# Optimization experiments

Hardware: AMD Instinct MI355X
Metric: run time of the kernel (lower is better)

The kernel has to match this reference:

```python
import jax, jax.numpy as jnp
import numpy as np

T, B, D, H = 1024, 8, 1024, 16
HD = D // H  # head_dim = 64


def setup_inputs() -> dict:
    key = jax.random.key(0)
    ks = jax.random.split(key, 11)
    s = 1.0 / np.sqrt(D)
    return {
        "query": jax.random.normal(ks[0], (T, B, D), jnp.float32),
        "key": jax.random.normal(ks[1], (T, B, D), jnp.float32),
        "value": jax.random.normal(ks[2], (T, B, D), jnp.float32),
        "Wq": jax.random.normal(ks[3], (D, D), jnp.float32) * s,
        "bq": jax.random.normal(ks[4], (D,), jnp.float32) * s,
        "Wk": jax.random.normal(ks[5], (D, D), jnp.float32) * s,
        "bk": jax.random.normal(ks[6], (D,), jnp.float32) * s,
        "Wv": jax.random.normal(ks[7], (D, D), jnp.float32) * s,
        "bv": jax.random.normal(ks[8], (D,), jnp.float32) * s,
        "Wo": jax.random.normal(ks[9], (D, D), jnp.float32) * s,
        "bo": jax.random.normal(ks[10], (D,), jnp.float32) * s,
    }


def reference(query, key, value, Wq, bq, Wk, bk, Wv, bv, Wo, bo):
    # query/key/value: (T, B, D) seq-first, as in nn.MultiheadAttention
    t, b, d = query.shape
    scale = HD ** -0.5
    # projections (torch Linear: x @ W.T + b), split into heads -> (B, H, T, HD)
    q = (query @ Wq.T + bq).reshape(t, b, H, HD).transpose(1, 2, 0, 3)
    k = (key @ Wk.T + bk).reshape(t, b, H, HD).transpose(1, 2, 0, 3)
    v = (value @ Wv.T + bv).reshape(t, b, H, HD).transpose(1, 2, 0, 3)
    # full (B, H, T, T) scores, matching the module's explicit materialization
    attn = jnp.einsum('bhtd,bhsd->bhts', q, k) * scale
    attn = jax.nn.softmax(attn, axis=-1)
    # (B, H, T, HD) -> (T, B, D)
    out = jnp.einsum('bhts,bhsd->bhtd', attn, v)
    out = out.transpose(2, 0, 1, 3).reshape(t, b, d)
    return out @ Wo.T + bo
```

## Files before the change

### kernel.cpp

```cpp
#include <hip/hip_runtime.h>

#define T_SEQ 1024
#define BATCH 8
#define DMODEL 1024
#define NHEAD 16
#define HDIM 64
#define M_ROWS (T_SEQ * BATCH)
#define QSCALE (0.125f * 1.44269504088896f)

typedef unsigned short ushort_t;
typedef __attribute__((ext_vector_type(8))) short short8;
typedef __attribute__((ext_vector_type(4))) float f32x4;

#define G2L16(g, l) __builtin_amdgcn_global_load_lds(                      \
    (const __attribute__((address_space(1))) void*)(g),                    \
    (__attribute__((address_space(3))) void*)(l), 16, 0, 0)

static __device__ __forceinline__ ushort_t f2bf(float f) {
    unsigned int u = __builtin_bit_cast(unsigned int, f);
    u += 0x7FFFu + ((u >> 16) & 1u);
    return (ushort_t)(u >> 16);
}

#if __has_builtin(__builtin_amdgcn_cvt_pk_bf16_f32)
typedef __attribute__((ext_vector_type(2))) __bf16 bf16x2_t;
static __device__ __forceinline__ unsigned pk2(float lo, float hi) {
    bf16x2_t r = __builtin_amdgcn_cvt_pk_bf16_f32(lo, hi);
    return __builtin_bit_cast(unsigned, r);
}
#else
static __device__ __forceinline__ unsigned pk2(float lo, float hi) {
    return (unsigned)f2bf(lo) | ((unsigned)f2bf(hi) << 16);
}
#endif

#if __has_builtin(__builtin_amdgcn_exp2f)
#define EXP2F(x) __builtin_amdgcn_exp2f(x)
#else
#define EXP2F(x) exp2f(x)
#endif

__global__ __launch_bounds__(256) void cast3_bf16(
    const float4* __restrict__ a, const float4* __restrict__ b,
    const float4* __restrict__ c,
    uint2* __restrict__ oa, uint2* __restrict__ ob, uint2* __restrict__ oc,
    int n4)
{
    int i = blockIdx.x * 256 + threadIdx.x;
    if (i >= n4) return;
    const float4* src = (blockIdx.y == 0) ? a : (blockIdx.y == 1) ? b : c;
    uint2* dst        = (blockIdx.y == 0) ? oa : (blockIdx.y == 1) ? ob : oc;
    float4 v = src[i];
    uint2 o; o.x = pk2(v.x, v.y); o.y = pk2(v.z, v.w);
    dst[i] = o;
}

__global__ __launch_bounds__(256) void cast4_bf16(
    const float4* __restrict__ a, const float4* __restrict__ b,
    const float4* __restrict__ c, const float4* __restrict__ d,
    uint2* __restrict__ oa, uint2* __restrict__ ob,
    uint2* __restrict__ oc, uint2* __restrict__ od,
    int n4)
{
    int i = blockIdx.x * 256 + threadIdx.x;
    if (i >= n4) return;
    const float4* src = (blockIdx.y == 0) ? a : (blockIdx.y == 1) ? b
                      : (blockIdx.y == 2) ? c : d;
    uint2* dst        = (blockIdx.y == 0) ? oa : (blockIdx.y == 1) ? ob
                      : (blockIdx.y == 2) ? oc : od;
    float4 v = src[i];
    uint2 o; o.x = pk2(v.x, v.y); o.y = pk2(v.z, v.w);
    dst[i] = o;
}

template<bool OUT_BF16>
__global__ __launch_bounds__(256) void gemm_bt_mfma(
    const ushort_t* __restrict__ A, const ushort_t* __restrict__ Wbase,
    const float* __restrict__ bias0, const float* __restrict__ bias1,
    const float* __restrict__ bias2, void* __restrict__ Yv,
    int N, int K, float scale0)
{
    __shared__ ushort_t As[128 * 64];
    __shared__ ushort_t Bs[128 * 64];

    const int tid  = threadIdx.x;
    const int lane = tid & 63;
    const int quad = lane >> 4;
    const int l16  = lane & 15;
    const int w    = tid >> 6;
    const int wm   = w >> 1;
    const int wn   = w & 1;
    const int bn   = blockIdx.x;
    const int bmg  = blockIdx.y;

    const int sel = bmg >> 6;
    const ushort_t* Wb = Wbase + (size_t)sel * N * K;
    const float* bias = (sel == 0) ? bias0 : (sel == 1) ? bias1 : bias2;
    const float scale = (sel == 0) ? scale0 : 1.0f;

    const int srow_in = lane >> 3;
    const int sch     = lane & 7;

    const f32x4 zero4 = {0.f, 0.f, 0.f, 0.f};
    f32x4 acc[4][4];
#pragma unroll
    for (int i = 0; i < 4; i++)
#pragma unroll
        for (int j = 0; j < 4; j++) acc[i][j] = zero4;

    for (int k0 = 0; k0 < K; k0 += 64) {
        __syncthreads();
#pragma unroll
        for (int u = 0; u < 4; u++) {
            int seg = w * 4 + u;
            int row = seg * 8 + srow_in;
            int chs = sch ^ (row & 7);
            G2L16(&A [(size_t)(bmg * 128 + row) * K + k0 + chs * 8],
                  (char*)As + seg * 1024);
            G2L16(&Wb[(size_t)(bn  * 128 + row) * K + k0 + chs * 8],
                  (char*)Bs + seg * 1024);
        }
        __syncthreads();

#pragma unroll
        for (int ks = 0; ks < 2; ks++) {
            short8 af[4], bfr[4];
#pragma unroll
            for (int i = 0; i < 4; i++) {
                int row = wm * 64 + i * 16 + l16;
                af[i] = *(const short8*)&As[row * 64 + (((ks * 4 + quad) ^ (row & 7)) * 8)];
            }
#pragma unroll
            for (int j = 0; j < 4; j++) {
                int row = wn * 64 + j * 16 + l16;
                bfr[j] = *(const short8*)&Bs[row * 64 + (((ks * 4 + quad) ^ (row & 7)) * 8)];
            }
#pragma unroll
            for (int i = 0; i < 4; i++)
#pragma unroll
                for (int j = 0; j < 4; j++)
                    acc[i][j] = __builtin_amdgcn_mfma_f32_16x16x32_bf16(
                        af[i], bfr[j], acc[i][j], 0, 0, 0);
        }
    }

    float bj[4];
#pragma unroll
    for (int j = 0; j < 4; j++) bj[j] = bias[bn * 128 + wn * 64 + j * 16 + l16];
#pragma unroll
    for (int i = 0; i < 4; i++) {
#pragma unroll
        for (int r = 0; r < 4; r++) {
            size_t row = (size_t)(bmg * 128 + wm * 64 + i * 16 + quad * 4 + r);
#pragma unroll
            for (int j = 0; j < 4; j++) {
                int col = bn * 128 + wn * 64 + j * 16 + l16;
                float v = (acc[i][j][r] + bj[j]) * scale;
                if (OUT_BF16) ((ushort_t*)Yv)[row * N + col] = f2bf(v);
                else          ((float*)   Yv)[row * N + col] = v;
            }
        }
    }
}

__global__ __launch_bounds__(256) void transpose_v(
    const ushort_t* __restrict__ Vp, ushort_t* __restrict__ Vt)
{
    __shared__ ushort_t Ts[64][72];
    const int tid = threadIdx.x;
    const int t0 = blockIdx.x * 64;
    const int bh = blockIdx.y;
    const int b = bh >> 4, h = bh & 15;

#pragma unroll
    for (int u = 0; u < 2; u++) {
        int e = u * 256 + tid;
        int row = e >> 3, ch = (e & 7) * 8;
        uint4 v = *(const uint4*)&Vp[((size_t)(t0 + row) * BATCH + b) * DMODEL + h * 64 + ch];
        *(uint4*)&Ts[row][ch] = v;
    }
    __syncthreads();
#pragma unroll
    for (int u = 0; u < 2; u++) {
        int e = u * 256 + tid;
        int d = e >> 3, tc = (e & 7) * 8;
        uint4 o;
        o.x = (unsigned)Ts[tc + 0][d] | ((unsigned)Ts[tc + 1][d] << 16);
        o.y = (unsigned)Ts[tc + 2][d] | ((unsigned)Ts[tc + 3][d] << 16);
        o.z = (unsigned)Ts[tc + 4][d] | ((unsigned)Ts[tc + 5][d] << 16);
        o.w = (unsigned)Ts[tc + 6][d] | ((unsigned)Ts[tc + 7][d] << 16);
        *(uint4*)&Vt[((size_t)(bh * 64 + d)) * T_SEQ + t0 + tc] = o;
    }
}

__global__ __launch_bounds__(256) void attn_mfma(
    const ushort_t* __restrict__ Qp, const ushort_t* __restrict__ Kp,
    const ushort_t* __restrict__ VtG, ushort_t* __restrict__ Ao)
{
    __shared__ ushort_t Ks[64 * 64];
    __shared__ ushort_t Vs[64 * 64];
    __shared__ ushort_t Pl[4][32][72];

    const int tid  = threadIdx.x;
    const int lane = tid & 63;
    const int w    = tid >> 6;
    const int quad = lane >> 4;
    const int l16  = lane & 15;
    const int bid  = blockIdx.x;
    const int qb   = bid >> 7;
    const int bh   = bid & 127;
    const int b    = bh >> 4, h = bh & 15;
    const int hoff = h * 64;
    const int q0   = qb * 128 + w * 32;

    const int srow_in = lane >> 3;
    const int sch     = lane & 7;

    short8 qf[2][2];
#pragma unroll
    for (int rt = 0; rt < 2; rt++)
#pragma unroll
        for (int ks = 0; ks < 2; ks++)
            qf[rt][ks] = *(const short8*)&Qp[((size_t)(q0 + rt * 16 + l16) * BATCH + b) * DMODEL
                                             + hoff + ks * 32 + quad * 8];

    short8 ones;
#pragma unroll
    for (int i = 0; i < 8; i++) ones[i] = (short)0x3F80;

    const f32x4 zero4 = {0.f, 0.f, 0.f, 0.f};
    f32x4 oacc[2][4], lacc[2];
#pragma unroll
    for (int rt = 0; rt < 2; rt++) {
        lacc[rt] = zero4;
#pragma unroll
        for (int c = 0; c < 4; c++) oacc[rt][c] = zero4;
    }

    for (int s0 = 0; s0 < T_SEQ; s0 += 64) {
        __syncthreads();
#pragma unroll
        for (int u = 0; u < 2; u++) {
            int seg = w * 2 + u;
            int row = seg * 8 + srow_in;
            int chs = sch ^ (row & 7);
            G2L16(&Kp[((size_t)(s0 + row) * BATCH + b) * DMODEL + hoff + chs * 8],
                  (char*)Ks + seg * 1024);
            G2L16(&VtG[((size_t)(bh * 64 + row)) * T_SEQ + s0 + chs * 8],
                  (char*)Vs + seg * 1024);
        }
        __syncthreads();

        f32x4 sacc[2][4];
#pragma unroll
        for (int rt = 0; rt < 2; rt++)
#pragma unroll
            for (int c = 0; c < 4; c++) sacc[rt][c] = zero4;
#pragma unroll
        for (int c = 0; c < 4; c++) {
            int row = c * 16 + l16;
#pragma unroll
            for (int ks = 0; ks < 2; ks++) {
                short8 kf = *(const short8*)&Ks[row * 64 + (((ks * 4 + quad) ^ (row & 7)) * 8)];
#pragma unroll
                for (int rt = 0; rt < 2; rt++)
                    sacc[rt][c] = __builtin_amdgcn_mfma_f32_16x16x32_bf16(
                        kf, qf[rt][ks], sacc[rt][c], 0, 0, 0);
            }
        }

#pragma unroll
        for (int rt = 0; rt < 2; rt++)
#pragma unroll
            for (int c = 0; c < 4; c++) {
                uint2 pv;
                pv.x = pk2(EXP2F(sacc[rt][c][0]), EXP2F(sacc[rt][c][1]));
                pv.y = pk2(EXP2F(sacc[rt][c][2]), EXP2F(sacc[rt][c][3]));
                *(uint2*)&Pl[w][rt * 16 + l16][c * 16 + quad * 4] = pv;
            }

        short8 pf[2][2];
#pragma unroll
        for (int rt = 0; rt < 2; rt++)
#pragma unroll
            for (int ks = 0; ks < 2; ks++)
                pf[rt][ks] = *(const short8*)&Pl[w][rt * 16 + l16][ks * 32 + quad * 8];

#pragma unroll
        for (int rt = 0; rt < 2; rt++)
#pragma unroll
            for (int ks = 0; ks < 2; ks++)
                lacc[rt] = __builtin_amdgcn_mfma_f32_16x16x32_bf16(
                    ones, pf[rt][ks], lacc[rt], 0, 0, 0);

#pragma unroll
        for (int dt = 0; dt < 4; dt++) {
            int row = dt * 16 + l16;
#pragma unroll
            for (int ks = 0; ks < 2; ks++) {
                short8 vf = *(const short8*)&Vs[row * 64 + (((ks * 4 + quad) ^ (row & 7)) * 8)];
#pragma unroll
                for (int rt = 0; rt < 2; rt++)
                    oacc[rt][dt] = __builtin_amdgcn_mfma_f32_16x16x32_bf16(
                        vf, pf[rt][ks], oacc[rt][dt], 0, 0, 0);
            }
        }
    }

#pragma unroll
    for (int rt = 0; rt < 2; rt++) {
        float inv = 1.f / lacc[rt][0];
#pragma unroll
        for (int dt = 0; dt < 4; dt++) {
            uint2 ov;
            ov.x = pk2(oacc[rt][dt][0] * inv, oacc[rt][dt][1] * inv);
            ov.y = pk2(oacc[rt][dt][2] * inv, oacc[rt][dt][3] * inv);
            *(uint2*)&Pl[w][rt * 16 + l16][dt * 16 + quad * 4] = ov;
        }
    }
#pragma unroll
    for (int it = 0; it < 4; it++) {
        int row = it * 8 + (lane >> 3);
        int ch  = lane & 7;
        uint4 val = *(const uint4*)&Pl[w][row][ch * 8];
        *(uint4*)&Ao[((size_t)(q0 + row) * BATCH + b) * DMODEL + hoff + ch * 8] = val;
    }
}

extern "C" void kernel_launch(void* const* d_in, const int* in_sizes, int n_in,
                              void* d_out, int out_size, void* d_ws, size_t ws_size,
                              hipStream_t stream)
{
    const float* q  = (const float*)d_in[0];
    const float* k  = (const float*)d_in[1];
    const float* v  = (const float*)d_in[2];
    const float* Wq = (const float*)d_in[3];
    const float* bq = (const float*)d_in[4];
    const float* Wk = (const float*)d_in[5];
    const float* bk = (const float*)d_in[6];
    const float* Wv = (const float*)d_in[7];
    const float* bv = (const float*)d_in[8];
    const float* Wo = (const float*)d_in[9];
    const float* bo = (const float*)d_in[10];

    ushort_t* ws = (ushort_t*)d_ws;
    const size_t E = (size_t)M_ROWS * DMODEL;
    const size_t EW = (size_t)DMODEL * DMODEL;
    ushort_t* qb  = ws;
    ushort_t* kb  = ws + E;
    ushort_t* vb  = ws + 2 * E;
    ushort_t* Qp  = ws + 3 * E;
    ushort_t* Kp  = ws + 4 * E;
    ushort_t* Vp  = ws + 5 * E;
    ushort_t* Wqb = ws + 6 * E;
    ushort_t* Wkb = Wqb + EW;
    ushort_t* Wvb = Wkb + EW;
    ushort_t* Wob = Wvb + EW;
    ushort_t* Vt  = qb;
    ushort_t* Aob = kb;

    const int n4_in = (int)(E / 4);
    const int n4_w  = (int)(EW / 4);
    cast3_bf16<<<dim3(n4_in / 256, 3), 256, 0, stream>>>(
        (const float4*)q, (const float4*)k, (const float4*)v,
        (uint2*)qb, (uint2*)kb, (uint2*)vb, n4_in);
    cast4_bf16<<<dim3(n4_w / 256, 4), 256, 0, stream>>>(
        (const float4*)Wq, (const float4*)Wk, (const float4*)Wv, (const float4*)Wo,
        (uint2*)Wqb, (uint2*)Wkb, (uint2*)Wvb, (uint2*)Wob, n4_w);

    gemm_bt_mfma<true><<<dim3(DMODEL / 128, 3 * M_ROWS / 128), 256, 0, stream>>>(
        qb, Wqb, bq, bk, bv, Qp, DMODEL, DMODEL, QSCALE);

    transpose_v<<<dim3(T_SEQ / 64, BATCH * NHEAD), 256, 0, stream>>>(Vp, Vt);

    attn_mfma<<<dim3(8 * 128), 256, 0, stream>>>(Qp, Kp, Vt, Aob);

    gemm_bt_mfma<false><<<dim3(DMODEL / 128, M_ROWS / 128), 256, 0, stream>>>(
        Aob, Wob, bo, bo, bo, d_out, DMODEL, DMODEL, 1.0f);
}
```

Measured before the change: 336.6 us.

## Double-buffer attention K/V tiles, merge cast kernels, remap GEMM block order

Attention now keeps two LDS buffers for K and V and issues the next tile's global-to-LDS loads before computing on the current one. It also raises wave priority around the MFMA sections, so load latency is hidden behind compute with one barrier per iteration instead of two. The two cast kernels become a single flat 1D launch, saving one launch. GEMM workgroup IDs are remapped so consecutive blocks are spread across XCDs, which changes cache locality. Costs are double the K/V LDS (possibly lower occupancy) and a hand-placed waitcnt/barrier scheme that must be exactly right.

```diff
diff --git a/kernel.cpp b/kernel.cpp
--- a/kernel.cpp
+++ b/kernel.cpp
@@ -8,6 +8,9 @@
 #define M_ROWS (T_SEQ * BATCH)
 #define QSCALE (0.125f * 1.44269504088896f)
 
+#define N4BIG   (M_ROWS * DMODEL / 4)
+#define N4SMALL (DMODEL * DMODEL / 4)
+
 typedef unsigned short ushort_t;
 typedef __attribute__((ext_vector_type(8))) short short8;
 typedef __attribute__((ext_vector_type(4))) float f32x4;
@@ -15,6 +18,10 @@
 #define G2L16(g, l) __builtin_amdgcn_global_load_lds(                      \
     (const __attribute__((address_space(1))) void*)(g),                    \
     (__attribute__((address_space(3))) void*)(l), 16, 0, 0)
+
+#define SBAR()   __builtin_amdgcn_s_barrier()
+#define LGKM0()  asm volatile("s_waitcnt lgkmcnt(0)" ::: "memory")
+#define SCHEDB() __builtin_amdgcn_sched_barrier(0)
 
 static __device__ __forceinline__ ushort_t f2bf(float f) {
     unsigned int u = __builtin_bit_cast(unsigned int, f);
@@ -40,37 +47,32 @@
 #define EXP2F(x) exp2f(x)
 #endif
 
-__global__ __launch_bounds__(256) void cast3_bf16(
-    const float4* __restrict__ a, const float4* __restrict__ b,
-    const float4* __restrict__ c,
-    uint2* __restrict__ oa, uint2* __restrict__ ob, uint2* __restrict__ oc,
-    int n4)
+__global__ __launch_bounds__(256) void cast_all_1d(
+    const float4* __restrict__ q, const float4* __restrict__ k,
+    const float4* __restrict__ v, const float4* __restrict__ wq,
+    const float4* __restrict__ wk, const float4* __restrict__ wv,
+    const float4* __restrict__ wo,
+    uint2* __restrict__ dq, uint2* __restrict__ dk, uint2* __restrict__ dv,
+    uint2* __restrict__ dwq, uint2* __restrict__ dwk, uint2* __restrict__ dwv,
+    uint2* __restrict__ dwo)
 {
-    int i = blockIdx.x * 256 + threadIdx.x;
-    if (i >= n4) return;
-    const float4* src = (blockIdx.y == 0) ? a : (blockIdx.y == 1) ? b : c;
-    uint2* dst        = (blockIdx.y == 0) ? oa : (blockIdx.y == 1) ? ob : oc;
-    float4 v = src[i];
-    uint2 o; o.x = pk2(v.x, v.y); o.y = pk2(v.z, v.w);
-    dst[i] = o;
-}
-
-__global__ __launch_bounds__(256) void cast4_bf16(
-    const float4* __restrict__ a, const float4* __restrict__ b,
-    const float4* __restrict__ c, const float4* __restrict__ d,
-    uint2* __restrict__ oa, uint2* __restrict__ ob,
-    uint2* __restrict__ oc, uint2* __restrict__ od,
-    int n4)
-{
-    int i = blockIdx.x * 256 + threadIdx.x;
-    if (i >= n4) return;
-    const float4* src = (blockIdx.y == 0) ? a : (blockIdx.y == 1) ? b
-                      : (blockIdx.y == 2) ? c : d;
-    uint2* dst        = (blockIdx.y == 0) ? oa : (blockIdx.y == 1) ? ob
-                      : (blockIdx.y == 2) ? oc : od;
-    float4 v = src[i];
-    uint2 o; o.x = pk2(v.x, v.y); o.y = pk2(v.z, v.w);
-    dst[i] = o;
+    const int i = blockIdx.x * 256 + threadIdx.x;
+    const float4* s; uint2* d; int off;
+    if (i < 3 * N4BIG) {
+        const int t = i >> 21;
+        off = i & (N4BIG - 1);
+        s = (t == 0) ? q : (t == 1) ? k : v;
+        d = (t == 0) ? dq : (t == 1) ? dk : dv;
+    } else {
+        const int j = i - 3 * N4BIG;
+        const int t = j >> 18;
+        off = j & (N4SMALL - 1);
+        s = (t == 0) ? wq : (t == 1) ? wk : (t == 2) ? wv : wo;
+        d = (t == 0) ? dwq : (t == 1) ? dwk : (t == 2) ? dwv : dwo;
+    }
+    float4 val = s[off];
+    uint2 o; o.x = pk2(val.x, val.y); o.y = pk2(val.z, val.w);
+    d[off] = o;
 }
 
 template<bool OUT_BF16>
@@ -90,8 +92,12 @@
     const int w    = tid >> 6;
     const int wm   = w >> 1;
     const int wn   = w & 1;
-    const int bn   = blockIdx.x;
-    const int bmg  = blockIdx.y;
+
+    const int nwg = gridDim.x * gridDim.y;
+    const int lin = blockIdx.y * gridDim.x + blockIdx.x;
+    const int t   = (lin & 7) * (nwg >> 3) + (lin >> 3);
+    const int bn  = t & 7;
+    const int bmg = t >> 3;
 
     const int sel = bmg >> 6;
     const ushort_t* Wb = Wbase + (size_t)sel * N * K;
@@ -197,8 +203,8 @@
     const ushort_t* __restrict__ Qp, const ushort_t* __restrict__ Kp,
     const ushort_t* __restrict__ VtG, ushort_t* __restrict__ Ao)
 {
-    __shared__ ushort_t Ks[64 * 64];
-    __shared__ ushort_t Vs[64 * 64];
+    __shared__ ushort_t Ks[2][64 * 64];
+    __shared__ ushort_t Vs[2][64 * 64];
     __shared__ ushort_t Pl[4][32][72];
 
     const int tid  = threadIdx.x;
@@ -237,37 +243,49 @@
         for (int c = 0; c < 4; c++) oacc[rt][c] = zero4;
     }
 
-    for (int s0 = 0; s0 < T_SEQ; s0 += 64) {
-        __syncthreads();
-#pragma unroll
-        for (int u = 0; u < 2; u++) {
-            int seg = w * 2 + u;
-            int row = seg * 8 + srow_in;
-            int chs = sch ^ (row & 7);
-            G2L16(&Kp[((size_t)(s0 + row) * BATCH + b) * DMODEL + hoff + chs * 8],
-                  (char*)Ks + seg * 1024);
-            G2L16(&VtG[((size_t)(bh * 64 + row)) * T_SEQ + s0 + chs * 8],
-                  (char*)Vs + seg * 1024);
-        }
-        __syncthreads();
+#define STAGE_KV(s0_, buf)                                                       \
+    do {                                                                         \
+        _Pragma("unroll")                                                        \
+        for (int u = 0; u < 2; u++) {                                            \
+            int seg = w * 2 + u;                                                 \
+            int row = seg * 8 + srow_in;                                         \
+            int chs = sch ^ (row & 7);                                           \
+            G2L16(&Kp[((size_t)((s0_) + row) * BATCH + b) * DMODEL + hoff + chs * 8], \
+                  (char*)&Ks[buf][0] + seg * 1024);                              \
+            G2L16(&VtG[((size_t)(bh * 64 + row)) * T_SEQ + (s0_) + chs * 8],     \
+                  (char*)&Vs[buf][0] + seg * 1024);                              \
+        }                                                                        \
+    } while (0)
+
+    STAGE_KV(0, 0);
+
+    for (int it = 0; it < 16; ++it) {
+        const int cur = it & 1;
+
+        asm volatile("s_waitcnt vmcnt(0)" ::: "memory");
+        SBAR();
+        SCHEDB();
+        if (it + 1 < 16) STAGE_KV((it + 1) * 64, cur ^ 1);
 
         f32x4 sacc[2][4];
 #pragma unroll
         for (int rt = 0; rt < 2; rt++)
 #pragma unroll
             for (int c = 0; c < 4; c++) sacc[rt][c] = zero4;
+        __builtin_amdgcn_s_setprio(1);
 #pragma unroll
         for (int c = 0; c < 4; c++) {
             int row = c * 16 + l16;
 #pragma unroll
             for (int ks = 0; ks < 2; ks++) {
-                short8 kf = *(const short8*)&Ks[row * 64 + (((ks * 4 + quad) ^ (row & 7)) * 8)];
+                short8 kf = *(const short8*)&Ks[cur][row * 64 + (((ks * 4 + quad) ^ (row & 7)) * 8)];
 #pragma unroll
                 for (int rt = 0; rt < 2; rt++)
                     sacc[rt][c] = __builtin_amdgcn_mfma_f32_16x16x32_bf16(
                         kf, qf[rt][ks], sacc[rt][c], 0, 0, 0);
             }
         }
+        __builtin_amdgcn_s_setprio(0);
 
 #pragma unroll
         for (int rt = 0; rt < 2; rt++)
@@ -293,19 +311,24 @@
                 lacc[rt] = __builtin_amdgcn_mfma_f32_16x16x32_bf16(
                     ones, pf[rt][ks], lacc[rt], 0, 0, 0);
 
+        __builtin_amdgcn_s_setprio(1);
 #pragma unroll
         for (int dt = 0; dt < 4; dt++) {
             int row = dt * 16 + l16;
 #pragma unroll
             for (int ks = 0; ks < 2; ks++) {
-                short8 vf = *(const short8*)&Vs[row * 64 + (((ks * 4 + quad) ^ (row & 7)) * 8)];
+                short8 vf = *(const short8*)&Vs[cur][row * 64 + (((ks * 4 + quad) ^ (row & 7)) * 8)];
 #pragma unroll
                 for (int rt = 0; rt < 2; rt++)
                     oacc[rt][dt] = __builtin_amdgcn_mfma_f32_16x16x32_bf16(
                         vf, pf[rt][ks], oacc[rt][dt], 0, 0, 0);
             }
         }
-    }
+        __builtin_amdgcn_s_setprio(0);
+
+        LGKM0();
+    }
+#undef STAGE_KV
 
 #pragma unroll
     for (int rt = 0; rt < 2; rt++) {
@@ -359,14 +382,12 @@
     ushort_t* Vt  = qb;
     ushort_t* Aob = kb;
 
-    const int n4_in = (int)(E / 4);
-    const int n4_w  = (int)(EW / 4);
-    cast3_bf16<<<dim3(n4_in / 256, 3), 256, 0, stream>>>(
+    const int ncast = (3 * N4BIG + 4 * N4SMALL) / 256;
+    cast_all_1d<<<dim3(ncast), 256, 0, stream>>>(
         (const float4*)q, (const float4*)k, (const float4*)v,
-        (uint2*)qb, (uint2*)kb, (uint2*)vb, n4_in);
-    cast4_bf16<<<dim3(n4_w / 256, 4), 256, 0, stream>>>(
         (const float4*)Wq, (const float4*)Wk, (const float4*)Wv, (const float4*)Wo,
-        (uint2*)Wqb, (uint2*)Wkb, (uint2*)Wvb, (uint2*)Wob, n4_w);
+        (uint2*)qb, (uint2*)kb, (uint2*)vb,
+        (uint2*)Wqb, (uint2*)Wkb, (uint2*)Wvb, (uint2*)Wob);
 
     gemm_bt_mfma<true><<<dim3(DMODEL / 128, 3 * M_ROWS / 128), 256, 0, stream>>>(
         qb, Wqb, bq, bk, bv, Qp, DMODEL, DMODEL, QSCALE);
```

Result: faster. 325.1 us (-3.4%).
